# Performance work log

Hardware: AMD Instinct MI355X
Metric: run time of the kernel (lower is better)

The kernel has to match this reference:

```python
import jax, jax.numpy as jnp
import numpy as np

B, C, H, W = 8, 128, 128, 128
HEADS = 8

def setup_inputs() -> dict:
    key = jax.random.key(0)
    k1, k2 = jax.random.split(key)
    x1 = jax.random.normal(k1, (B, C, H, W), dtype=jnp.float32)
    x2 = jax.random.normal(k2, (B, C, H, W), dtype=jnp.float32)
    return {"x1": x1, "x2": x2}

def reference(x1, x2):
    b, c, h, w = x1.shape
    n = h * w
    hk = c // HEADS  # head key channels
    hv = c // HEADS  # head value channels
    # [B,C,N] layouts (channels-first, as in torch after transpose back)
    vals = x1.reshape(b, c, n)   # values come from x1
    kq = x2.reshape(b, c, n)     # keys and queries come from x2
    k = kq.reshape(b, HEADS, hk, n)
    v = vals.reshape(b, HEADS, hv, n)
    key_sm = jax.nn.softmax(k, axis=-1)   # softmax over N (torch dim=2)
    query_sm = jax.nn.softmax(k, axis=2)  # softmax over head channels (torch dim=1)
    # context = key @ value^T : [B,h,hk,hv]
    context = jnp.einsum('bhkn,bhvn->bhkv', key_sm, v)
    # attended = context^T @ query : [B,h,hv,N]
    attended = jnp.einsum('bhkv,bhkn->bhvn', context, query_sm)
    return attended.reshape(b, c, H, W)
```

## Files before the change

kernel.cpp:

```cpp
#include <hip/hip_runtime.h>
#include <math.h>

#define N_     16384
#define N4     4096
#define BHN    64
#define CH     16
#define CHUNKS 32

#define WS_PART 0
#define WS_ZP   (BHN * CHUNKS * 256)

typedef __attribute__((ext_vector_type(8))) short short8;
typedef __attribute__((ext_vector_type(4))) float f32x4;

static __device__ inline short f2bf(float f) {
    __bf16 b = (__bf16)f;
    return __builtin_bit_cast(short, b);
}

__global__ __launch_bounds__(256) void k_ctx_mfma(const float* __restrict__ x1,
                                                  const float* __restrict__ x2,
                                                  float* __restrict__ ws) {
    int chunk = blockIdx.x;
    int bh    = blockIdx.y;
    int tid   = threadIdx.x;
    int w = tid >> 6, l = tid & 63;
    int row16 = l & 15;
    int n0 = chunk * 512 + w * 128;

    const float4* pk = (const float4*)(x2 + (size_t)(bh * CH + row16) * N_ + n0)
                       + (l >> 4) * 2;
    const float4* pv = (const float4*)(x1 + (size_t)(bh * CH + row16) * N_ + n0)
                       + (l >> 4) * 2;

    float4 ka[8], va[8];
    #pragma unroll
    for (int s = 0; s < 4; ++s) {
        ka[2 * s]     = pk[s * 8];
        ka[2 * s + 1] = pk[s * 8 + 1];
    }
    #pragma unroll
    for (int s = 0; s < 4; ++s) {
        va[2 * s]     = pv[s * 8];
        va[2 * s + 1] = pv[s * 8 + 1];
    }

    f32x4 acc = {0.f, 0.f, 0.f, 0.f};
    float zacc = 0.f;

    #pragma unroll
    for (int s = 0; s < 4; ++s) {
        float4 k0 = ka[2 * s], k1 = ka[2 * s + 1];
        float4 v0 = va[2 * s], v1 = va[2 * s + 1];
        float e0 = __expf(k0.x), e1 = __expf(k0.y), e2 = __expf(k0.z), e3 = __expf(k0.w);
        float e4 = __expf(k1.x), e5 = __expf(k1.y), e6 = __expf(k1.z), e7 = __expf(k1.w);
        zacc += ((e0 + e1) + (e2 + e3)) + ((e4 + e5) + (e6 + e7));
        short8 af = {f2bf(e0), f2bf(e1), f2bf(e2), f2bf(e3),
                     f2bf(e4), f2bf(e5), f2bf(e6), f2bf(e7)};
        short8 bf = {f2bf(v0.x), f2bf(v0.y), f2bf(v0.z), f2bf(v0.w),
                     f2bf(v1.x), f2bf(v1.y), f2bf(v1.z), f2bf(v1.w)};
        acc = __builtin_amdgcn_mfma_f32_16x16x32_bf16(af, bf, acc, 0, 0, 0);
    }

    __shared__ float cred[4][256];
    __shared__ float zred[4][16];

    float z = zacc;
    z += __shfl_xor(z, 16);
    z += __shfl_xor(z, 32);
    if (l < 16) zred[w][l] = z;

    #pragma unroll
    for (int r = 0; r < 4; ++r)
        cred[w][((l >> 4) * 4 + r) * 16 + row16] = acc[r];
    __syncthreads();

    if (tid < 16) {
        float zz = (zred[0][tid] + zred[1][tid]) + (zred[2][tid] + zred[3][tid]);
        ws[WS_ZP + (bh * CHUNKS + chunk) * 16 + tid] = zz;
    }
    float c = (cred[0][tid] + cred[1][tid]) + (cred[2][tid] + cred[3][tid]);
    ws[WS_PART + (size_t)(bh * CHUNKS + chunk) * 256 + tid] = c;
}

__global__ __launch_bounds__(256) void k_attend(const float* __restrict__ x2,
                                                const float* __restrict__ ws,
                                                float* __restrict__ out) {
    int cb  = blockIdx.x;
    int bh  = blockIdx.y;
    int tid = threadIdx.x;

    __shared__ float q_s[16][256];
    __shared__ float ctxs[256];
    __shared__ float rzs[16];

    float csum = 0.f;
    #pragma unroll
    for (int c = 0; c < CHUNKS; ++c)
        csum += ws[WS_PART + (size_t)(bh * CHUNKS + c) * 256 + tid];
    if (tid < 16) {
        float z = 0.f;
        #pragma unroll
        for (int c = 0; c < CHUNKS; ++c)
            z += ws[WS_ZP + (bh * CHUNKS + c) * 16 + tid];
        rzs[tid] = 1.0f / z;
    }

    const float4* px = (const float4*)(x2 + (size_t)bh * CH * N_);
    int base4 = cb * 64;
    #pragma unroll
    for (int r = 0; r < 4; ++r) {
        int idx = r * 256 + tid;
        int ch = idx >> 6, j = idx & 63;
        float4 v = px[(size_t)ch * N4 + base4 + j];
        *(float4*)&q_s[ch][j * 4] = v;
    }
    __syncthreads();

    ctxs[tid] = csum * rzs[tid >> 4];

    {
        int col = tid;
        float kv[16];
        #pragma unroll
        for (int c = 0; c < 16; ++c) kv[c] = q_s[c][col];
        float mx = kv[0];
        #pragma unroll
        for (int c = 1; c < 16; ++c) mx = fmaxf(mx, kv[c]);
        float s = 0.f;
        #pragma unroll
        for (int c = 0; c < 16; ++c) { kv[c] = __expf(kv[c] - mx); s += kv[c]; }
        float rs = 1.0f / s;
        #pragma unroll
        for (int c = 0; c < 16; ++c) q_s[c][col] = kv[c] * rs;
    }
    __syncthreads();

    int vg = tid >> 6, cq = tid & 63;
    int vv0 = vg * 4, c0 = cq * 4;
    float4 a0 = make_float4(0.f,0.f,0.f,0.f);
    float4 a1 = a0, a2 = a0, a3 = a0;
    #pragma unroll
    for (int kk = 0; kk < 16; ++kk) {
        float4 cx = *(const float4*)&ctxs[kk * 16 + vv0];
        float4 q4 = *(const float4*)&q_s[kk][c0];
        a0.x = fmaf(q4.x, cx.x, a0.x); a0.y = fmaf(q4.x, cx.y, a0.y);
        a0.z = fmaf(q4.x, cx.z, a0.z); a0.w = fmaf(q4.x, cx.w, a0.w);
        a1.x = fmaf(q4.y, cx.x, a1.x); a1.y = fmaf(q4.y, cx.y, a1.y);
        a1.z = fmaf(q4.y, cx.z, a1.z); a1.w = fmaf(q4.y, cx.w, a1.w);
        a2.x = fmaf(q4.z, cx.x, a2.x); a2.y = fmaf(q4.z, cx.y, a2.y);
        a2.z = fmaf(q4.z, cx.z, a2.z); a2.w = fmaf(q4.z, cx.w, a2.w);
        a3.x = fmaf(q4.w, cx.x, a3.x); a3.y = fmaf(q4.w, cx.y, a3.y);
        a3.z = fmaf(q4.w, cx.z, a3.z); a3.w = fmaf(q4.w, cx.w, a3.w);
    }
    size_t outbase = (size_t)bh * CH * N_ + (size_t)cb * 256 + c0;
    float4 o;
    o = make_float4(a0.x, a1.x, a2.x, a3.x);
    *(float4*)&out[outbase + (size_t)(vv0 + 0) * N_] = o;
    o = make_float4(a0.y, a1.y, a2.y, a3.y);
    *(float4*)&out[outbase + (size_t)(vv0 + 1) * N_] = o;
    o = make_float4(a0.z, a1.z, a2.z, a3.z);
    *(float4*)&out[outbase + (size_t)(vv0 + 2) * N_] = o;
    o = make_float4(a0.w, a1.w, a2.w, a3.w);
    *(float4*)&out[outbase + (size_t)(vv0 + 3) * N_] = o;
}

extern "C" void kernel_launch(void* const* d_in, const int* in_sizes, int n_in,
                              void* d_out, int out_size, void* d_ws, size_t ws_size,
                              hipStream_t stream) {
    const float* x1 = (const float*)d_in[0];
    const float* x2 = (const float*)d_in[1];
    float* out = (float*)d_out;
    float* ws  = (float*)d_ws;

    k_ctx_mfma <<<dim3(CHUNKS, BHN), 256, 0, stream>>>(x1, x2, ws);
    k_attend   <<<dim3(64, BHN),     256, 0, stream>>>(x2, ws, out);
}
```

Measured before the change: 51.78 us.

## Double-buffer context kernel loads via global_load_lds with swizzled LDS and fewer chunks

```diff
diff --git a/kernel.cpp b/kernel.cpp
--- a/kernel.cpp
+++ b/kernel.cpp
@@ -5,7 +5,7 @@
 #define N4     4096
 #define BHN    64
 #define CH     16
-#define CHUNKS 32
+#define CHUNKS 16
 
 #define WS_PART 0
 #define WS_ZP   (BHN * CHUNKS * 256)
@@ -13,66 +13,91 @@
 typedef __attribute__((ext_vector_type(8))) short short8;
 typedef __attribute__((ext_vector_type(4))) float f32x4;
 
-static __device__ inline short f2bf(float f) {
+static __device__ __forceinline__ short f2bf(float f) {
     __bf16 b = (__bf16)f;
     return __builtin_bit_cast(short, b);
 }
 
-__global__ __launch_bounds__(256) void k_ctx_mfma(const float* __restrict__ x1,
-                                                  const float* __restrict__ x2,
-                                                  float* __restrict__ ws) {
+static __device__ __forceinline__ void gload16(const float* g, float* l) {
+    __builtin_amdgcn_global_load_lds(
+        (const __attribute__((address_space(1))) unsigned int*)g,
+        (__attribute__((address_space(3))) unsigned int*)l, 16, 0, 0);
+}
+
+__global__ __launch_bounds__(256, 4) void k_ctx_mfma(const float* __restrict__ x1,
+                                                     const float* __restrict__ x2,
+                                                     float* __restrict__ ws) {
     int chunk = blockIdx.x;
     int bh    = blockIdx.y;
     int tid   = threadIdx.x;
     int w = tid >> 6, l = tid & 63;
-    int row16 = l & 15;
-    int n0 = chunk * 512 + w * 128;
-
-    const float4* pk = (const float4*)(x2 + (size_t)(bh * CH + row16) * N_ + n0)
-                       + (l >> 4) * 2;
-    const float4* pv = (const float4*)(x1 + (size_t)(bh * CH + row16) * N_ + n0)
-                       + (l >> 4) * 2;
-
-    float4 ka[8], va[8];
-    #pragma unroll
-    for (int s = 0; s < 4; ++s) {
-        ka[2 * s]     = pk[s * 8];
-        ka[2 * s + 1] = pk[s * 8 + 1];
-    }
-    #pragma unroll
-    for (int s = 0; s < 4; ++s) {
-        va[2 * s]     = pv[s * 8];
-        va[2 * s + 1] = pv[s * 8 + 1];
-    }
+
+    __shared__ float ka_s[2][16 * 128];
+    __shared__ float va_s[2][16 * 128];
+    __shared__ float cred[4][256];
+    __shared__ float zred[4][16];
+
+    int half = l >> 5;
+    int u    = l & 31;
+    int rowA = 4 * w + half;
+    int rowB = 4 * w + 2 + half;
+    int vA = u ^ ((rowA & 7) << 1);
+    int vB = u ^ ((rowB & 7) << 1);
+    const float* gk0 = x2 + (size_t)(bh * CH + rowA) * N_ + chunk * 1024 + vA * 4;
+    const float* gk1 = x2 + (size_t)(bh * CH + rowB) * N_ + chunk * 1024 + vB * 4;
+    const float* gv0 = x1 + (size_t)(bh * CH + rowA) * N_ + chunk * 1024 + vA * 4;
+    const float* gv1 = x1 + (size_t)(bh * CH + rowB) * N_ + chunk * 1024 + vB * 4;
+
+    int row  = l & 15;
+    int v0   = w * 8 + (l >> 4) * 2;
+    int u0   = v0 ^ ((row & 7) << 1);
+    int offr = row * 128 + u0 * 4;
 
     f32x4 acc = {0.f, 0.f, 0.f, 0.f};
     float zacc = 0.f;
 
-    #pragma unroll
-    for (int s = 0; s < 4; ++s) {
-        float4 k0 = ka[2 * s], k1 = ka[2 * s + 1];
-        float4 v0 = va[2 * s], v1 = va[2 * s + 1];
-        float e0 = __expf(k0.x), e1 = __expf(k0.y), e2 = __expf(k0.z), e3 = __expf(k0.w);
-        float e4 = __expf(k1.x), e5 = __expf(k1.y), e6 = __expf(k1.z), e7 = __expf(k1.w);
+#define STAGE(b, t) do {                                         \
+        gload16(gk0 + (t) * 128, &ka_s[b][(2 * w)     * 256]);   \
+        gload16(gk1 + (t) * 128, &ka_s[b][(2 * w + 1) * 256]);   \
+        gload16(gv0 + (t) * 128, &va_s[b][(2 * w)     * 256]);   \
+        gload16(gv1 + (t) * 128, &va_s[b][(2 * w + 1) * 256]);   \
+    } while (0)
+
+    STAGE(0, 0);
+    asm volatile("s_waitcnt vmcnt(0)" ::: "memory");
+    __syncthreads();
+
+    for (int t = 0; t < 8; ++t) {
+        int b = t & 1;
+        if (t < 7) STAGE(1 - b, t + 1);
+
+        float4 kq0 = *(const float4*)&ka_s[b][offr];
+        float4 kq1 = *(const float4*)&ka_s[b][offr + 4];
+        float4 vq0 = *(const float4*)&va_s[b][offr];
+        float4 vq1 = *(const float4*)&va_s[b][offr + 4];
+        float e0 = __expf(kq0.x), e1 = __expf(kq0.y), e2 = __expf(kq0.z), e3 = __expf(kq0.w);
+        float e4 = __expf(kq1.x), e5 = __expf(kq1.y), e6 = __expf(kq1.z), e7 = __expf(kq1.w);
         zacc += ((e0 + e1) + (e2 + e3)) + ((e4 + e5) + (e6 + e7));
         short8 af = {f2bf(e0), f2bf(e1), f2bf(e2), f2bf(e3),
                      f2bf(e4), f2bf(e5), f2bf(e6), f2bf(e7)};
-        short8 bf = {f2bf(v0.x), f2bf(v0.y), f2bf(v0.z), f2bf(v0.w),
-                     f2bf(v1.x), f2bf(v1.y), f2bf(v1.z), f2bf(v1.w)};
-        acc = __builtin_amdgcn_mfma_f32_16x16x32_bf16(af, bf, acc, 0, 0, 0);
-    }
-
-    __shared__ float cred[4][256];
-    __shared__ float zred[4][16];
-
-    float z = zacc;
-    z += __shfl_xor(z, 16);
-    z += __shfl_xor(z, 32);
-    if (l < 16) zred[w][l] = z;
+        short8 bv = {f2bf(vq0.x), f2bf(vq0.y), f2bf(vq0.z), f2bf(vq0.w),
+                     f2bf(vq1.x), f2bf(vq1.y), f2bf(vq1.z), f2bf(vq1.w)};
+        acc = __builtin_amdgcn_mfma_f32_16x16x32_bf16(af, bv, acc, 0, 0, 0);
+
+        if (t < 7) {
+            asm volatile("s_waitcnt vmcnt(0)" ::: "memory");
+            __syncthreads();
+        }
+    }
+#undef STAGE
+
+    zacc += __shfl_xor(zacc, 16);
+    zacc += __shfl_xor(zacc, 32);
+    if (l < 16) zred[w][l] = zacc;
 
     #pragma unroll
     for (int r = 0; r < 4; ++r)
-        cred[w][((l >> 4) * 4 + r) * 16 + row16] = acc[r];
+        cred[w][((l >> 4) * 4 + r) * 16 + row] = acc[r];
     __syncthreads();
 
     if (tid < 16) {
```

Measured after the change: 51.40 us. No clear change (-0.7%).

## Add separate context reduction kernel and stage ctx chunks through LDS

Applied to the files above, without the earlier changes.

```diff
diff --git a/kernel.cpp b/kernel.cpp
--- a/kernel.cpp
+++ b/kernel.cpp
@@ -5,15 +5,16 @@
 #define N4     4096
 #define BHN    64
 #define CH     16
-#define CHUNKS 32
+#define CHUNKS 64
 
 #define WS_PART 0
 #define WS_ZP   (BHN * CHUNKS * 256)
+#define WS_CTX  (WS_ZP + BHN * CHUNKS * 16)
 
 typedef __attribute__((ext_vector_type(8))) short short8;
 typedef __attribute__((ext_vector_type(4))) float f32x4;
 
-static __device__ inline short f2bf(float f) {
+static __device__ __forceinline__ short f2bf(float f) {
     __bf16 b = (__bf16)f;
     return __builtin_bit_cast(short, b);
 }
@@ -25,54 +26,63 @@
     int bh    = blockIdx.y;
     int tid   = threadIdx.x;
     int w = tid >> 6, l = tid & 63;
-    int row16 = l & 15;
-    int n0 = chunk * 512 + w * 128;
-
-    const float4* pk = (const float4*)(x2 + (size_t)(bh * CH + row16) * N_ + n0)
-                       + (l >> 4) * 2;
-    const float4* pv = (const float4*)(x1 + (size_t)(bh * CH + row16) * N_ + n0)
-                       + (l >> 4) * 2;
-
-    float4 ka[8], va[8];
-    #pragma unroll
-    for (int s = 0; s < 4; ++s) {
-        ka[2 * s]     = pk[s * 8];
-        ka[2 * s + 1] = pk[s * 8 + 1];
-    }
-    #pragma unroll
-    for (int s = 0; s < 4; ++s) {
-        va[2 * s]     = pv[s * 8];
-        va[2 * s + 1] = pv[s * 8 + 1];
-    }
-
+
+    __shared__ float ka_s[16][260];
+    __shared__ float va_s[16][260];
+    __shared__ float cred[4][256];
+    __shared__ float zred[4][16];
+
+    const float4* px2 = (const float4*)(x2 + (size_t)bh * CH * N_);
+    const float4* px1 = (const float4*)(x1 + (size_t)bh * CH * N_);
+    int base4 = chunk * 64;
+
+    float4 kq[4], vq[4];
+    #pragma unroll
+    for (int r = 0; r < 4; ++r) {
+        int idx = r * 256 + tid;
+        kq[r] = px2[(size_t)(idx >> 6) * N4 + base4 + (idx & 63)];
+    }
+    #pragma unroll
+    for (int r = 0; r < 4; ++r) {
+        int idx = r * 256 + tid;
+        vq[r] = px1[(size_t)(idx >> 6) * N4 + base4 + (idx & 63)];
+    }
+    #pragma unroll
+    for (int r = 0; r < 4; ++r) {
+        int idx = r * 256 + tid;
+        int row = idx >> 6, j = idx & 63;
+        *(float4*)&ka_s[row][j * 4] = kq[r];
+        *(float4*)&va_s[row][j * 4] = vq[r];
+    }
+    __syncthreads();
+
+    int row = l & 15;
     f32x4 acc = {0.f, 0.f, 0.f, 0.f};
     float zacc = 0.f;
-
-    #pragma unroll
-    for (int s = 0; s < 4; ++s) {
-        float4 k0 = ka[2 * s], k1 = ka[2 * s + 1];
-        float4 v0 = va[2 * s], v1 = va[2 * s + 1];
+    #pragma unroll
+    for (int s = 0; s < 2; ++s) {
+        int col = (2 * w + s) * 32 + (l >> 4) * 8;
+        float4 k0 = *(const float4*)&ka_s[row][col];
+        float4 k1 = *(const float4*)&ka_s[row][col + 4];
+        float4 v0 = *(const float4*)&va_s[row][col];
+        float4 v1 = *(const float4*)&va_s[row][col + 4];
         float e0 = __expf(k0.x), e1 = __expf(k0.y), e2 = __expf(k0.z), e3 = __expf(k0.w);
         float e4 = __expf(k1.x), e5 = __expf(k1.y), e6 = __expf(k1.z), e7 = __expf(k1.w);
         zacc += ((e0 + e1) + (e2 + e3)) + ((e4 + e5) + (e6 + e7));
         short8 af = {f2bf(e0), f2bf(e1), f2bf(e2), f2bf(e3),
                      f2bf(e4), f2bf(e5), f2bf(e6), f2bf(e7)};
-        short8 bf = {f2bf(v0.x), f2bf(v0.y), f2bf(v0.z), f2bf(v0.w),
+        short8 bv = {f2bf(v0.x), f2bf(v0.y), f2bf(v0.z), f2bf(v0.w),
                      f2bf(v1.x), f2bf(v1.y), f2bf(v1.z), f2bf(v1.w)};
-        acc = __builtin_amdgcn_mfma_f32_16x16x32_bf16(af, bf, acc, 0, 0, 0);
-    }
-
-    __shared__ float cred[4][256];
-    __shared__ float zred[4][16];
-
-    float z = zacc;
-    z += __shfl_xor(z, 16);
-    z += __shfl_xor(z, 32);
-    if (l < 16) zred[w][l] = z;
+        acc = __builtin_amdgcn_mfma_f32_16x16x32_bf16(af, bv, acc, 0, 0, 0);
+    }
+
+    zacc += __shfl_xor(zacc, 16);
+    zacc += __shfl_xor(zacc, 32);
+    if (l < 16) zred[w][l] = zacc;
 
     #pragma unroll
     for (int r = 0; r < 4; ++r)
-        cred[w][((l >> 4) * 4 + r) * 16 + row16] = acc[r];
+        cred[w][((l >> 4) * 4 + r) * 16 + row] = acc[r];
     __syncthreads();
 
     if (tid < 16) {
@@ -81,6 +91,36 @@
     }
     float c = (cred[0][tid] + cred[1][tid]) + (cred[2][tid] + cred[3][tid]);
     ws[WS_PART + (size_t)(bh * CHUNKS + chunk) * 256 + tid] = c;
+}
+
+__global__ __launch_bounds__(1024) void k_reduce(float* __restrict__ ws) {
+    int bh  = blockIdx.x;
+    int tid = threadIdx.x;
+    int p = tid & 255, q = tid >> 8;
+
+    float s = 0.f;
+    #pragma unroll
+    for (int c = q; c < CHUNKS; c += 4)
+        s += ws[WS_PART + (size_t)(bh * CHUNKS + c) * 256 + p];
+
+    __shared__ float red[4][256];
+    __shared__ float zpart[4][16];
+    red[q][p] = s;
+    if (p < 16) {
+        float z = 0.f;
+        #pragma unroll
+        for (int c = q; c < CHUNKS; c += 4)
+            z += ws[WS_ZP + (bh * CHUNKS + c) * 16 + p];
+        zpart[q][p] = z;
+    }
+    __syncthreads();
+
+    if (tid < 256) {
+        float tot = (red[0][p] + red[1][p]) + (red[2][p] + red[3][p]);
+        int kk = p >> 4;
+        float zz = (zpart[0][kk] + zpart[1][kk]) + (zpart[2][kk] + zpart[3][kk]);
+        ws[WS_CTX + bh * 256 + p] = tot / zz;
+    }
 }
 
 __global__ __launch_bounds__(256) void k_attend(const float* __restrict__ x2,
@@ -92,19 +132,8 @@
 
     __shared__ float q_s[16][256];
     __shared__ float ctxs[256];
-    __shared__ float rzs[16];
-
-    float csum = 0.f;
-    #pragma unroll
-    for (int c = 0; c < CHUNKS; ++c)
-        csum += ws[WS_PART + (size_t)(bh * CHUNKS + c) * 256 + tid];
-    if (tid < 16) {
-        float z = 0.f;
-        #pragma unroll
-        for (int c = 0; c < CHUNKS; ++c)
-            z += ws[WS_ZP + (bh * CHUNKS + c) * 16 + tid];
-        rzs[tid] = 1.0f / z;
-    }
+
+    ctxs[tid] = ws[WS_CTX + bh * 256 + tid];
 
     const float4* px = (const float4*)(x2 + (size_t)bh * CH * N_);
     int base4 = cb * 64;
@@ -116,8 +145,6 @@
         *(float4*)&q_s[ch][j * 4] = v;
     }
     __syncthreads();
-
-    ctxs[tid] = csum * rzs[tid >> 4];
 
     {
         int col = tid;
@@ -173,6 +200,7 @@
     float* out = (float*)d_out;
     float* ws  = (float*)d_ws;
 
-    k_ctx_mfma <<<dim3(CHUNKS, BHN), 256, 0, stream>>>(x1, x2, ws);
-    k_attend   <<<dim3(64, BHN),     256, 0, stream>>>(x2, ws, out);
-}
+    k_ctx_mfma <<<dim3(CHUNKS, BHN), 256,  0, stream>>>(x1, x2, ws);
+    k_reduce   <<<BHN,               1024, 0, stream>>>(ws);
+    k_attend   <<<dim3(64, BHN),     256,  0, stream>>>(x2, ws, out);
+}
```

Result: slower. 63.61 us (+22.9%).

## Stage bf16 exp-keys and values through LDS with coalesced row loads, halve chunks

Applied to the files above, without the earlier changes.

```diff
diff --git a/kernel.cpp b/kernel.cpp
--- a/kernel.cpp
+++ b/kernel.cpp
@@ -5,7 +5,7 @@
 #define N4     4096
 #define BHN    64
 #define CH     16
-#define CHUNKS 32
+#define CHUNKS 16
 
 #define WS_PART 0
 #define WS_ZP   (BHN * CHUNKS * 256)
@@ -13,7 +13,7 @@
 typedef __attribute__((ext_vector_type(8))) short short8;
 typedef __attribute__((ext_vector_type(4))) float f32x4;
 
-static __device__ inline short f2bf(float f) {
+static __device__ __forceinline__ short f2bf(float f) {
     __bf16 b = (__bf16)f;
     return __builtin_bit_cast(short, b);
 }
@@ -25,60 +25,84 @@
     int bh    = blockIdx.y;
     int tid   = threadIdx.x;
     int w = tid >> 6, l = tid & 63;
+
+    __shared__ __align__(16) short e_s[16][1032];
+    __shared__ __align__(16) short v_s[16][1032];
+    __shared__ float cred[4][256];
+    __shared__ float zs[16];
+
+    const float* xb2 = x2 + (size_t)bh * CH * N_ + chunk * 1024;
+    const float* xb1 = x1 + (size_t)bh * CH * N_ + chunk * 1024;
+
+    {
+        int row = 4 * w;
+        const float4* src = (const float4*)(xb2 + (size_t)row * N_);
+        float4 a0 = src[l], a1 = src[64 + l], a2 = src[128 + l], a3 = src[192 + l];
+        #pragma unroll
+        for (int rr = 0; rr < 4; ++rr) {
+            float4 b0 = a0, b1 = a1, b2 = a2, b3 = a3;
+            if (rr < 3) {
+                const float4* nx = (const float4*)(xb2 + (size_t)(row + rr + 1) * N_);
+                a0 = nx[l]; a1 = nx[64 + l]; a2 = nx[128 + l]; a3 = nx[192 + l];
+            }
+            int r = row + rr;
+            float e[16];
+            e[0]=__expf(b0.x); e[1]=__expf(b0.y); e[2]=__expf(b0.z); e[3]=__expf(b0.w);
+            e[4]=__expf(b1.x); e[5]=__expf(b1.y); e[6]=__expf(b1.z); e[7]=__expf(b1.w);
+            e[8]=__expf(b2.x); e[9]=__expf(b2.y); e[10]=__expf(b2.z); e[11]=__expf(b2.w);
+            e[12]=__expf(b3.x); e[13]=__expf(b3.y); e[14]=__expf(b3.z); e[15]=__expf(b3.w);
+            float z = 0.f;
+            #pragma unroll
+            for (int i = 0; i < 16; ++i) z += e[i];
+            #pragma unroll
+            for (int off = 1; off < 64; off <<= 1) z += __shfl_xor(z, off);
+            if (l == 0) zs[r] = z;
+            #pragma unroll
+            for (int s = 0; s < 4; ++s) {
+                short4 pk = make_short4(f2bf(e[s*4]), f2bf(e[s*4+1]),
+                                        f2bf(e[s*4+2]), f2bf(e[s*4+3]));
+                *(short4*)&e_s[r][s * 256 + l * 4] = pk;
+            }
+        }
+    }
+    {
+        int row = 4 * w;
+        const float4* src = (const float4*)(xb1 + (size_t)row * N_);
+        float4 a0 = src[l], a1 = src[64 + l], a2 = src[128 + l], a3 = src[192 + l];
+        #pragma unroll
+        for (int rr = 0; rr < 4; ++rr) {
+            float4 b0 = a0, b1 = a1, b2 = a2, b3 = a3;
+            if (rr < 3) {
+                const float4* nx = (const float4*)(xb1 + (size_t)(row + rr + 1) * N_);
+                a0 = nx[l]; a1 = nx[64 + l]; a2 = nx[128 + l]; a3 = nx[192 + l];
+            }
+            int r = row + rr;
+            *(short4*)&v_s[r][0 * 256 + l * 4] = make_short4(f2bf(b0.x), f2bf(b0.y), f2bf(b0.z), f2bf(b0.w));
+            *(short4*)&v_s[r][1 * 256 + l * 4] = make_short4(f2bf(b1.x), f2bf(b1.y), f2bf(b1.z), f2bf(b1.w));
+            *(short4*)&v_s[r][2 * 256 + l * 4] = make_short4(f2bf(b2.x), f2bf(b2.y), f2bf(b2.z), f2bf(b2.w));
+            *(short4*)&v_s[r][3 * 256 + l * 4] = make_short4(f2bf(b3.x), f2bf(b3.y), f2bf(b3.z), f2bf(b3.w));
+        }
+    }
+    __syncthreads();
+
     int row16 = l & 15;
-    int n0 = chunk * 512 + w * 128;
-
-    const float4* pk = (const float4*)(x2 + (size_t)(bh * CH + row16) * N_ + n0)
-                       + (l >> 4) * 2;
-    const float4* pv = (const float4*)(x1 + (size_t)(bh * CH + row16) * N_ + n0)
-                       + (l >> 4) * 2;
-
-    float4 ka[8], va[8];
-    #pragma unroll
-    for (int s = 0; s < 4; ++s) {
-        ka[2 * s]     = pk[s * 8];
-        ka[2 * s + 1] = pk[s * 8 + 1];
-    }
-    #pragma unroll
-    for (int s = 0; s < 4; ++s) {
-        va[2 * s]     = pv[s * 8];
-        va[2 * s + 1] = pv[s * 8 + 1];
-    }
-
+    int q     = l >> 4;
     f32x4 acc = {0.f, 0.f, 0.f, 0.f};
-    float zacc = 0.f;
-
-    #pragma unroll
-    for (int s = 0; s < 4; ++s) {
-        float4 k0 = ka[2 * s], k1 = ka[2 * s + 1];
-        float4 v0 = va[2 * s], v1 = va[2 * s + 1];
-        float e0 = __expf(k0.x), e1 = __expf(k0.y), e2 = __expf(k0.z), e3 = __expf(k0.w);
-        float e4 = __expf(k1.x), e5 = __expf(k1.y), e6 = __expf(k1.z), e7 = __expf(k1.w);
-        zacc += ((e0 + e1) + (e2 + e3)) + ((e4 + e5) + (e6 + e7));
-        short8 af = {f2bf(e0), f2bf(e1), f2bf(e2), f2bf(e3),
-                     f2bf(e4), f2bf(e5), f2bf(e6), f2bf(e7)};
-        short8 bf = {f2bf(v0.x), f2bf(v0.y), f2bf(v0.z), f2bf(v0.w),
-                     f2bf(v1.x), f2bf(v1.y), f2bf(v1.z), f2bf(v1.w)};
-        acc = __builtin_amdgcn_mfma_f32_16x16x32_bf16(af, bf, acc, 0, 0, 0);
-    }
-
-    __shared__ float cred[4][256];
-    __shared__ float zred[4][16];
-
-    float z = zacc;
-    z += __shfl_xor(z, 16);
-    z += __shfl_xor(z, 32);
-    if (l < 16) zred[w][l] = z;
+    #pragma unroll
+    for (int s = 0; s < 8; ++s) {
+        int col = w * 256 + s * 32 + q * 8;
+        short8 af = *(const short8*)&e_s[row16][col];
+        short8 bv = *(const short8*)&v_s[row16][col];
+        acc = __builtin_amdgcn_mfma_f32_16x16x32_bf16(af, bv, acc, 0, 0, 0);
+    }
 
     #pragma unroll
     for (int r = 0; r < 4; ++r)
-        cred[w][((l >> 4) * 4 + r) * 16 + row16] = acc[r];
-    __syncthreads();
-
-    if (tid < 16) {
-        float zz = (zred[0][tid] + zred[1][tid]) + (zred[2][tid] + zred[3][tid]);
-        ws[WS_ZP + (bh * CHUNKS + chunk) * 16 + tid] = zz;
-    }
+        cred[w][(q * 4 + r) * 16 + row16] = acc[r];
+    __syncthreads();
+
+    if (tid < 16)
+        ws[WS_ZP + (bh * CHUNKS + chunk) * 16 + tid] = zs[tid];
     float c = (cred[0][tid] + cred[1][tid]) + (cred[2][tid] + cred[3][tid]);
     ws[WS_PART + (size_t)(bh * CHUNKS + chunk) * 256 + tid] = c;
 }
```

Result: no change. 52.03 us (+0.5%).
